# Kernel optimization log

Hardware: AMD Instinct MI355X
Metric: run time of the kernel (lower is better)

The kernel has to match this reference:

```python
import jax, jax.numpy as jnp
import numpy as np

# Hardcoded hyperparameters from the torch module
E = 128   # n_embd
H = 4     # n_head
HS = 32   # head_size = n_embd // n_head
L = 4     # n_layer
T = 512   # block_size (full context)
V = 512   # vocab_size (quantization_levels)
B = 64    # batch
SCALE = 0.02  # init std per _init_weights


def _ln(x, g, b):
    mu = x.mean(-1, keepdims=True)
    var = ((x - mu) ** 2).mean(-1, keepdims=True)
    return (x - mu) / jnp.sqrt(var + 1e-5) * g + b


def setup_inputs() -> dict:
    key = jax.random.key(0)
    ks = jax.random.split(key, 24)
    rn = lambda k, shape: SCALE * jax.random.normal(k, shape, dtype=jnp.float32)
    return {
        "idx": jax.random.randint(ks[0], (B, T), 0, V),
        "tok_emb": rn(ks[1], (V, E)),
        "pos_emb": rn(ks[2], (T, E)),
        # per-head projections, stacked over layers and heads: x[...,E] @ wq[l,h] -> [...,HS]
        "wq": rn(ks[3], (L, H, E, HS)),
        "wk": rn(ks[4], (L, H, E, HS)),
        "wv": rn(ks[5], (L, H, E, HS)),
        "w_proj": rn(ks[6], (L, E, E)),   # torch Linear weight layout [out, in]
        "b_proj": jnp.zeros((L, E), jnp.float32),
        "ln1_g": jnp.ones((L, E), jnp.float32),
        "ln1_b": jnp.zeros((L, E), jnp.float32),
        "ln2_g": jnp.ones((L, E), jnp.float32),
        "ln2_b": jnp.zeros((L, E), jnp.float32),
        "w1": rn(ks[7], (L, 4 * E, E)),
        "b1": jnp.zeros((L, 4 * E), jnp.float32),
        "w2": rn(ks[8], (L, E, 4 * E)),
        "b2": jnp.zeros((L, E), jnp.float32),
        "lnf_g": jnp.ones((E,), jnp.float32),
        "lnf_b": jnp.zeros((E,), jnp.float32),
        "w_head": rn(ks[9], (V, E)),
        "b_head": jnp.zeros((V,), jnp.float32),
    }


def reference(idx, tok_emb, pos_emb, wq, wk, wv, w_proj, b_proj,
              ln1_g, ln1_b, ln2_g, ln2_b, w1, b1, w2, b2,
              lnf_g, lnf_b, w_head, b_head):
    Bv, Tv = idx.shape
    x = tok_emb[idx] + pos_emb[None, :Tv, :]          # [B,T,E]
    causal = jnp.tril(jnp.ones((Tv, Tv), dtype=bool))
    for l in range(L):
        h = _ln(x, ln1_g[l], ln1_b[l])
        q = jnp.einsum('bte,hed->bhtd', h, wq[l])     # [B,H,T,HS]
        k = jnp.einsum('bte,hed->bhtd', h, wk[l])
        v = jnp.einsum('bte,hed->bhtd', h, wv[l])
        s = jnp.einsum('bhtd,bhsd->bhts', q, k) * (HS ** -0.5)
        s = jnp.where(causal, s, -jnp.inf)
        a = jax.nn.softmax(s, axis=-1)
        o = jnp.einsum('bhts,bhsd->bhtd', a, v)       # [B,H,T,HS]
        o = o.transpose(0, 2, 1, 3).reshape(Bv, Tv, E)  # concat heads
        x = x + o @ w_proj[l].T + b_proj[l]
        h = _ln(x, ln2_g[l], ln2_b[l])
        x = x + jax.nn.gelu(h @ w1[l].T + b1[l], approximate=False) @ w2[l].T + b2[l]
    x = _ln(x, lnf_g, lnf_b)
    logits = x @ w_head.T + b_head                    # [B,T,V]
    return logits
```

## Files before the change

kernel.cpp:

```cpp
#include <hip/hip_runtime.h>

typedef __bf16 bf16x8 __attribute__((ext_vector_type(8)));
typedef __bf16 bf16x2 __attribute__((ext_vector_type(2)));
typedef float f32x4 __attribute__((ext_vector_type(4)));

constexpr int E_ = 128, H_ = 4, HS_ = 32, L_ = 4, T_ = 512, V_ = 512, B_ = 64;
constexpr int M_ = B_ * T_;

__device__ __forceinline__ float b2f(ushort u) {
    return __uint_as_float(((uint)u) << 16);
}
__device__ __forceinline__ ushort f2b(float f) {
    uint x = __float_as_uint(f);
    uint r = (x + 0x7fffu + ((x >> 16) & 1u)) >> 16;
    return (ushort)r;
}
__device__ __forceinline__ uint packbf(float a, float b) {
    bf16x2 t; t[0] = (__bf16)a; t[1] = (__bf16)b;
    return __builtin_bit_cast(uint, t);
}

__global__ void k_detect(const uint* __restrict__ ln1g_raw, int* __restrict__ flag) {
    if (threadIdx.x == 0 && blockIdx.x == 0)
        *flag = (ln1g_raw[0] == 0x3F800000u) ? 1 : 0;
}

constexpr int kNSeg = 19;
constexpr int kOffs[kNSeg + 1] = {
    0, 65536, 131072, 196608, 262144, 327680, 393216, 393728, 394240, 394752,
    395264, 395776, 657920, 659968, 922112, 922624, 922752, 922880, 988416, 988928
};
constexpr int kTotal = 988928;

struct SrcPtrs { const void* p[kNSeg]; };

__global__ __launch_bounds__(256) void k_convert(SrcPtrs sp, const int* __restrict__ flag,
                                                 ushort* __restrict__ arena) {
    int gid = blockIdx.x * 256 + threadIdx.x;
    if (gid >= kTotal) return;
    int s = 0;
    #pragma unroll
    for (int i = 1; i < kNSeg; i++) if (gid >= kOffs[i]) s = i;
    int local = gid - kOffs[s];
    ushort v;
    if (*flag) v = f2b(((const float*)sp.p[s])[local]);
    else       v = ((const ushort*)sp.p[s])[local];
    arena[gid] = v;
}

__global__ void k_prep_qkv(const ushort* __restrict__ wq, const ushort* __restrict__ wk,
                           const ushort* __restrict__ wv, ushort* __restrict__ wt) {
    int gid = blockIdx.x * 256 + threadIdx.x;
    if (gid >= L_ * 384 * E_) return;
    int e = gid & 127;
    int n = (gid >> 7) % 384;
    int l = gid / (384 * E_);
    int part = n >> 7, within = n & 127, hh = within >> 5, d = within & 31;
    const ushort* src = part == 0 ? wq : (part == 1 ? wk : wv);
    wt[gid] = src[(((size_t)(l * H_ + hh) * E_) + e) * HS_ + d];
}

__global__ __launch_bounds__(256) void k_embed_ln(const int* __restrict__ idx,
                                                  const ushort* __restrict__ tok,
                                                  const ushort* __restrict__ pos,
                                                  const ushort* __restrict__ g,
                                                  const ushort* __restrict__ beta,
                                                  float* __restrict__ x, ushort* __restrict__ h) {
    int wave = threadIdx.x >> 6, lane = threadIdx.x & 63;
    int row = blockIdx.x * 4 + wave;
    int t = row & (T_ - 1);
    int id = idx[row];
    float v0 = b2f(tok[id * E_ + lane])      + b2f(pos[t * E_ + lane]);
    float v1 = b2f(tok[id * E_ + lane + 64]) + b2f(pos[t * E_ + lane + 64]);
    size_t o = (size_t)row * E_;
    x[o + lane] = v0; x[o + lane + 64] = v1;
    float s = v0 + v1;
    #pragma unroll
    for (int m = 32; m; m >>= 1) s += __shfl_xor(s, m, 64);
    float mu = s * (1.0f / 128.0f);
    float d0 = v0 - mu, d1 = v1 - mu;
    float ss = d0 * d0 + d1 * d1;
    #pragma unroll
    for (int m = 32; m; m >>= 1) ss += __shfl_xor(ss, m, 64);
    float rstd = rsqrtf(ss * (1.0f / 128.0f) + 1e-5f);
    h[o + lane]      = f2b(d0 * rstd * b2f(g[lane])      + b2f(beta[lane]));
    h[o + lane + 64] = f2b(d1 * rstd * b2f(g[lane + 64]) + b2f(beta[lane + 64]));
}

template<int EPI>
__global__ __launch_bounds__(256) void k_gemm(const ushort* __restrict__ A, const ushort* __restrict__ W,
                                              const ushort* __restrict__ bias, void* __restrict__ outp,
                                              void* __restrict__ outp2,
                                              const ushort* __restrict__ lng, const ushort* __restrict__ lnb,
                                              const int* __restrict__ oflag, int K, int lda, int ldc) {
    int wid = threadIdx.x >> 6, lane = threadIdx.x & 63;
    int wr = wid >> 1, wc = wid & 1;
    int bm = blockIdx.x, bn = blockIdx.y;
    int r16 = lane & 15, kq = lane >> 4;
    const ushort* Abase = A + (size_t)(bm * 128 + wr * 64 + r16) * lda + kq * 8;
    const ushort* Wbase = W + (size_t)(bn * 128 + wc * 64 + r16) * K + kq * 8;
    bool f32out = false;
    if constexpr (EPI == 1) f32out = (*oflag != 0);
    f32x4 acc[4][4];
    #pragma unroll
    for (int i = 0; i < 4; i++)
        #pragma unroll
        for (int j = 0; j < 4; j++) acc[i][j] = (f32x4)0.0f;
    for (int k0 = 0; k0 < K; k0 += 32) {
        bf16x8 af[4], wf[4];
        #pragma unroll
        for (int mi = 0; mi < 4; mi++)
            af[mi] = *(const bf16x8*)(Abase + (size_t)mi * 16 * lda + k0);
        #pragma unroll
        for (int ni = 0; ni < 4; ni++)
            wf[ni] = *(const bf16x8*)(Wbase + (size_t)ni * 16 * K + k0);
        #pragma unroll
        for (int mi = 0; mi < 4; mi++)
            #pragma unroll
            for (int ni = 0; ni < 4; ni++)
                acc[mi][ni] = __builtin_amdgcn_mfma_f32_16x16x32_bf16(af[mi], wf[ni], acc[mi][ni], 0, 0, 0);
    }
    int orow0 = bm * 128 + wr * 64 + kq * 4;
    int ocol0 = bn * 128 + wc * 64 + r16;
    if constexpr (EPI == 5) {
        __shared__ float lnS[2][128], lnQ[2][128];
        float*  xg = (float*)outp;
        ushort* hg = (ushort*)outp2;
        #pragma unroll
        for (int ni = 0; ni < 4; ni++) {
            int col = ocol0 + ni * 16;
            float bv = b2f(bias[col]);
            #pragma unroll
            for (int mi = 0; mi < 4; mi++) {
                #pragma unroll
                for (int e = 0; e < 4; e++) {
                    size_t gi = (size_t)(orow0 + mi * 16 + e) * 128 + col;
                    float xv = xg[gi] + acc[mi][ni][e] + bv;
                    xg[gi] = xv;
                    acc[mi][ni][e] = xv;
                }
            }
        }
        #pragma unroll
        for (int mi = 0; mi < 4; mi++) {
            #pragma unroll
            for (int e = 0; e < 4; e++) {
                float s = 0.f, q = 0.f;
                #pragma unroll
                for (int ni = 0; ni < 4; ni++) { float v = acc[mi][ni][e]; s += v; q += v * v; }
                #pragma unroll
                for (int mk = 1; mk < 16; mk <<= 1) {
                    s += __shfl_xor(s, mk, 64); q += __shfl_xor(q, mk, 64);
                }
                if (r16 == 0) {
                    int lrow = wr * 64 + mi * 16 + kq * 4 + e;
                    lnS[wc][lrow] = s; lnQ[wc][lrow] = q;
                }
            }
        }
        __syncthreads();
        float gc[4], bc[4];
        #pragma unroll
        for (int ni = 0; ni < 4; ni++) {
            int col = ocol0 + ni * 16;
            gc[ni] = b2f(lng[col]); bc[ni] = b2f(lnb[col]);
        }
        #pragma unroll
        for (int mi = 0; mi < 4; mi++) {
            #pragma unroll
            for (int e = 0; e < 4; e++) {
                int lrow = wr * 64 + mi * 16 + kq * 4 + e;
                float tot = lnS[0][lrow] + lnS[1][lrow];
                float tq  = lnQ[0][lrow] + lnQ[1][lrow];
                float mu  = tot * (1.0f / 128.0f);
                float var = tq * (1.0f / 128.0f) - mu * mu;
                float rstd = rsqrtf(var + 1e-5f);
                size_t grow = (size_t)(bm * 128 + lrow) * 128;
                #pragma unroll
                for (int ni = 0; ni < 4; ni++) {
                    int col = ocol0 + ni * 16;
                    hg[grow + col] = f2b((acc[mi][ni][e] - mu) * rstd * gc[ni] + bc[ni]);
                }
            }
        }
        return;
    }
    if constexpr (EPI == 4) {
        if (bn == 2) {
            ushort* vt = (ushort*)outp2;
            #pragma unroll
            for (int mi = 0; mi < 4; mi++) {
                int row0 = orow0 + mi * 16;
                int bb = row0 >> 9, tt = row0 & 511;
                #pragma unroll
                for (int ni = 0; ni < 4; ni++) {
                    int vd = (ocol0 - 256) + ni * 16;
                    int hh = vd >> 5, dd = vd & 31;
                    ushort4 pk;
                    pk.x = f2b(acc[mi][ni][0]); pk.y = f2b(acc[mi][ni][1]);
                    pk.z = f2b(acc[mi][ni][2]); pk.w = f2b(acc[mi][ni][3]);
                    *(ushort4*)(vt + (((size_t)(bb * 4 + hh) * 32 + dd) << 9) + tt) = pk;
                }
            }
            return;
        }
    }
    #pragma unroll
    for (int mi = 0; mi < 4; mi++) {
        #pragma unroll
        for (int ni = 0; ni < 4; ni++) {
            int col = ocol0 + ni * 16;
            float bv = 0.0f;
            if constexpr (EPI == 1 || EPI == 2) bv = b2f(bias[col]);
            #pragma unroll
            for (int e = 0; e < 4; e++) {
                int row = orow0 + mi * 16 + e;
                float v = acc[mi][ni][e] + bv;
                if constexpr (EPI == 2) v = 0.5f * v * (1.0f + erff(v * 0.70710678118f));
                if constexpr (EPI == 1) {
                    if (f32out) ((float*)outp)[(size_t)row * ldc + col] = v;
                    else        ((ushort*)outp)[(size_t)row * ldc + col] = f2b(v);
                } else {
                    ((ushort*)outp)[(size_t)row * ldc + col] = f2b(v);
                }
            }
        }
    }
}

constexpr float SC_ = 0.2550348637f;

struct AST { f32x4 o0, o1; float m2, l; };

__device__ __forceinline__ void attn_step(AST& st, const f32x4& s0, const f32x4& s1,
                                          int j0, int myq, int r16, int g,
                                          const bf16x8& vf0, const bf16x8& vf1) {
    float sv[8];
    #pragma unroll
    for (int e = 0; e < 4; e++) {
        int ja = j0 + 4 * g + e;
        sv[e]     = (ja      <= myq) ? s0[e] * SC_ : -INFINITY;
        sv[4 + e] = (ja + 16 <= myq) ? s1[e] * SC_ : -INFINITY;
    }
    float pm = sv[0];
    #pragma unroll
    for (int i = 1; i < 8; i++) pm = fmaxf(pm, sv[i]);
    pm = fmaxf(pm, __shfl_xor(pm, 16, 64));
    pm = fmaxf(pm, __shfl_xor(pm, 32, 64));
    float mn = fmaxf(st.m2, pm);
    float c = exp2f(st.m2 - mn);
    float p[8], ps = 0.0f;
    #pragma unroll
    for (int i = 0; i < 8; i++) { p[i] = exp2f(sv[i] - mn); ps += p[i]; }
    ps += __shfl_xor(ps, 16, 64);
    ps += __shfl_xor(ps, 32, 64);
    st.l = st.l * c + ps;
    #pragma unroll
    for (int e = 0; e < 4; e++) { st.o0[e] *= c; st.o1[e] *= c; }
    st.m2 = mn;
    uint pk00 = packbf(p[0], p[1]), pk01 = packbf(p[2], p[3]);
    uint pk10 = packbf(p[4], p[5]), pk11 = packbf(p[6], p[7]);
    int ga = ((g & 1) << 5) + r16;
    int gb = ga + 16;
    uint A0 = (uint)__shfl((int)pk00, ga), A1 = (uint)__shfl((int)pk01, ga);
    uint C0 = (uint)__shfl((int)pk00, gb), C1 = (uint)__shfl((int)pk01, gb);
    uint B0 = (uint)__shfl((int)pk10, ga), B1 = (uint)__shfl((int)pk11, ga);
    uint D0 = (uint)__shfl((int)pk10, gb), D1 = (uint)__shfl((int)pk11, gb);
    bool hi2 = g >= 2;
    uint4 pr;
    pr.x = hi2 ? B0 : A0; pr.y = hi2 ? B1 : A1;
    pr.z = hi2 ? D0 : C0; pr.w = hi2 ? D1 : C1;
    bf16x8 pf = __builtin_bit_cast(bf16x8, pr);
    st.o0 = __builtin_amdgcn_mfma_f32_16x16x32_bf16(vf0, pf, st.o0, 0, 0, 0);
    st.o1 = __builtin_amdgcn_mfma_f32_16x16x32_bf16(vf1, pf, st.o1, 0, 0, 0);
}

__global__ __launch_bounds__(256) void k_attn_mfma(const ushort* __restrict__ qk,
                                                   const ushort* __restrict__ vt,
                                                   ushort* __restrict__ o) {
    int lane = threadIdx.x & 63, w = threadIdx.x >> 6;
    int qs = blockIdx.x, bh = blockIdx.y;
    int b = bh >> 2, h = bh & 3;
    int r16 = lane & 15, g = lane >> 4;
    int iA = qs * 4 + w;
    int qbaseA = iA * 16, qbaseB = (31 - iA) * 16;
    int myqA = qbaseA + r16, myqB = qbaseB + r16;
    int qmaxA = qbaseA + 15, qmaxB = qbaseB + 15;
    const ushort* qkbase = qk + (size_t)b * 512 * 256;
    bf16x8 qfA = *(const bf16x8*)(qkbase + (size_t)(qbaseA + r16) * 256 + h * 32 + g * 8);
    bf16x8 qfB = *(const bf16x8*)(qkbase + (size_t)(qbaseB + r16) * 256 + h * 32 + g * 8);
    const ushort* kptr = qkbase + 128 + h * 32 + g * 8;
    const ushort* vbase = vt + ((size_t)bh * 32) * 512;
    AST sA, sB;
    sA.o0 = (f32x4)0.0f; sA.o1 = (f32x4)0.0f; sA.m2 = -INFINITY; sA.l = 0.0f;
    sB = sA;
    for (int j0 = 0; j0 <= qmaxB; j0 += 32) {
        bf16x8 kf0 = *(const bf16x8*)(kptr + (size_t)(j0 + r16) * 256);
        bf16x8 kf1 = *(const bf16x8*)(kptr + (size_t)(j0 + 16 + r16) * 256);
        bf16x8 vf0 = *(const bf16x8*)(vbase + (size_t)r16 * 512 + j0 + g * 8);
        bf16x8 vf1 = *(const bf16x8*)(vbase + (size_t)(16 + r16) * 512 + j0 + g * 8);
        f32x4 b0 = __builtin_amdgcn_mfma_f32_16x16x32_bf16(kf0, qfB, (f32x4)0.0f, 0, 0, 0);
        f32x4 b1 = __builtin_amdgcn_mfma_f32_16x16x32_bf16(kf1, qfB, (f32x4)0.0f, 0, 0, 0);
        attn_step(sB, b0, b1, j0, myqB, r16, g, vf0, vf1);
        if (j0 <= qmaxA) {
            f32x4 a0 = __builtin_amdgcn_mfma_f32_16x16x32_bf16(kf0, qfA, (f32x4)0.0f, 0, 0, 0);
            f32x4 a1 = __builtin_amdgcn_mfma_f32_16x16x32_bf16(kf1, qfA, (f32x4)0.0f, 0, 0, 0);
            attn_step(sA, a0, a1, j0, myqA, r16, g, vf0, vf1);
        }
    }
    #pragma unroll
    for (int s = 0; s < 2; s++) {
        AST& st = s ? sB : sA;
        int qb = s ? qbaseB : qbaseA;
        float inv = 1.0f / st.l;
        ushort4 w0, w1;
        w0.x = f2b(st.o0[0] * inv); w0.y = f2b(st.o0[1] * inv);
        w0.z = f2b(st.o0[2] * inv); w0.w = f2b(st.o0[3] * inv);
        w1.x = f2b(st.o1[0] * inv); w1.y = f2b(st.o1[1] * inv);
        w1.z = f2b(st.o1[2] * inv); w1.w = f2b(st.o1[3] * inv);
        size_t orow = (size_t)(b * 512 + qb + r16) * 128 + h * 32;
        *(ushort4*)(o + orow + g * 4)      = w0;
        *(ushort4*)(o + orow + 16 + g * 4) = w1;
    }
}

extern "C" void kernel_launch(void* const* d_in, const int* in_sizes, int n_in,
                              void* d_out, int out_size, void* d_ws, size_t ws_size,
                              hipStream_t stream) {
    const int* idx = (const int*)d_in[0];

    char* ws = (char*)d_ws;
    float*  x     = (float*) (ws + 0);
    ushort* h     = (ushort*)(ws + (16u << 20));
    ushort* wqkvt = (ushort*)(ws + (24u << 20));
    ushort* arena = (ushort*)(ws + (25u << 20));
    int*    flag  = (int*)   (ws + (27u << 20));

    ushort* qkv = (ushort*)d_out;
    ushort* o   = (ushort*)d_out + (8u << 20);
    ushort* vt  = (ushort*)d_out + (12u << 20);
    ushort* mid = (ushort*)d_out;

    const ushort* tok    = arena + kOffs[0];
    const ushort* pos    = arena + kOffs[1];
    const ushort* wqp    = arena + kOffs[2];
    const ushort* wkp    = arena + kOffs[3];
    const ushort* wvp    = arena + kOffs[4];
    const ushort* w_proj = arena + kOffs[5];
    const ushort* b_proj = arena + kOffs[6];
    const ushort* ln1_g  = arena + kOffs[7];
    const ushort* ln1_b  = arena + kOffs[8];
    const ushort* ln2_g  = arena + kOffs[9];
    const ushort* ln2_b  = arena + kOffs[10];
    const ushort* w1     = arena + kOffs[11];
    const ushort* b1     = arena + kOffs[12];
    const ushort* w2     = arena + kOffs[13];
    const ushort* b2     = arena + kOffs[14];
    const ushort* lnf_g  = arena + kOffs[15];
    const ushort* lnf_b  = arena + kOffs[16];
    const ushort* w_head = arena + kOffs[17];
    const ushort* b_head = arena + kOffs[18];

    k_detect<<<1, 64, 0, stream>>>((const uint*)d_in[8], flag);
    SrcPtrs sp;
    for (int i = 0; i < kNSeg; i++) sp.p[i] = d_in[i + 1];
    k_convert<<<(kTotal + 255) / 256, 256, 0, stream>>>(sp, flag, arena);

    k_prep_qkv<<<768, 256, 0, stream>>>(wqp, wkp, wvp, wqkvt);
    k_embed_ln<<<M_ / 4, 256, 0, stream>>>(idx, tok, pos, ln1_g, ln1_b, x, h);
    for (int l = 0; l < L_; l++) {
        const ushort* ng = (l < 3) ? (ln1_g + (l + 1) * E_) : lnf_g;
        const ushort* nb = (l < 3) ? (ln1_b + (l + 1) * E_) : lnf_b;
        k_gemm<4><<<dim3(M_ / 128, 3), 256, 0, stream>>>(h, wqkvt + (size_t)l * 384 * E_, nullptr,
                                                         qkv, vt, nullptr, nullptr, nullptr, 128, 128, 256);
        k_attn_mfma<<<dim3(4, 256), 256, 0, stream>>>(qkv, vt, o);
        k_gemm<5><<<dim3(M_ / 128, 1), 256, 0, stream>>>(o, w_proj + (size_t)l * E_ * E_, b_proj + l * E_,
                                                         x, h, ln2_g + l * E_, ln2_b + l * E_, nullptr, 128, 128, 128);
        k_gemm<2><<<dim3(M_ / 128, 4), 256, 0, stream>>>(h, w1 + (size_t)l * 4 * E_ * E_, b1 + l * 4 * E_,
                                                         mid, nullptr, nullptr, nullptr, nullptr, 128, 128, 512);
        k_gemm<5><<<dim3(M_ / 128, 1), 256, 0, stream>>>(mid, w2 + (size_t)l * E_ * 4 * E_, b2 + l * E_,
                                                         x, h, ng, nb, nullptr, 512, 512, 128);
    }
    k_gemm<1><<<dim3(M_ / 128, 4), 256, 0, stream>>>(h, w_head, b_head, d_out, nullptr,
                                                     nullptr, nullptr, flag, 128, 128, 512);
}
```

Measured before the change: 524.6 us.

## Use two-pass attention softmax with precomputed row max and drop detect kernel

Attention now runs a first pass of QK^T MFMAs to find the exact row max, then a second pass computes exp, row sum and PV without the online rescaling of the accumulators. This removes per-step correction exponentials, accumulator scaling and max shuffles, at the cost of computing QK^T twice. The separate dtype-detect kernel is also removed; the convert and head GEMM kernels read the raw ln1_g word directly.

```diff
diff --git a/kernel.cpp b/kernel.cpp
--- a/kernel.cpp
+++ b/kernel.cpp
@@ -18,11 +18,6 @@
 __device__ __forceinline__ uint packbf(float a, float b) {
     bf16x2 t; t[0] = (__bf16)a; t[1] = (__bf16)b;
     return __builtin_bit_cast(uint, t);
-}
-
-__global__ void k_detect(const uint* __restrict__ ln1g_raw, int* __restrict__ flag) {
-    if (threadIdx.x == 0 && blockIdx.x == 0)
-        *flag = (ln1g_raw[0] == 0x3F800000u) ? 1 : 0;
 }
 
 constexpr int kNSeg = 19;
@@ -34,16 +29,16 @@
 
 struct SrcPtrs { const void* p[kNSeg]; };
 
-__global__ __launch_bounds__(256) void k_convert(SrcPtrs sp, const int* __restrict__ flag,
-                                                 ushort* __restrict__ arena) {
+__global__ __launch_bounds__(256) void k_convert(SrcPtrs sp, ushort* __restrict__ arena) {
     int gid = blockIdx.x * 256 + threadIdx.x;
     if (gid >= kTotal) return;
+    bool isf32 = (((const uint*)sp.p[7])[0] == 0x3F800000u);
     int s = 0;
     #pragma unroll
     for (int i = 1; i < kNSeg; i++) if (gid >= kOffs[i]) s = i;
     int local = gid - kOffs[s];
     ushort v;
-    if (*flag) v = f2b(((const float*)sp.p[s])[local]);
+    if (isf32) v = f2b(((const float*)sp.p[s])[local]);
     else       v = ((const ushort*)sp.p[s])[local];
     arena[gid] = v;
 }
@@ -92,7 +87,7 @@
                                               const ushort* __restrict__ bias, void* __restrict__ outp,
                                               void* __restrict__ outp2,
                                               const ushort* __restrict__ lng, const ushort* __restrict__ lnb,
-                                              const int* __restrict__ oflag, int K, int lda, int ldc) {
+                                              const uint* __restrict__ dtraw, int K, int lda, int ldc) {
     int wid = threadIdx.x >> 6, lane = threadIdx.x & 63;
     int wr = wid >> 1, wc = wid & 1;
     int bm = blockIdx.x, bn = blockIdx.y;
@@ -100,7 +95,7 @@
     const ushort* Abase = A + (size_t)(bm * 128 + wr * 64 + r16) * lda + kq * 8;
     const ushort* Wbase = W + (size_t)(bn * 128 + wc * 64 + r16) * K + kq * 8;
     bool f32out = false;
-    if constexpr (EPI == 1) f32out = (*oflag != 0);
+    if constexpr (EPI == 1) f32out = (dtraw[0] == 0x3F800000u);
     f32x4 acc[4][4];
     #pragma unroll
     for (int i = 0; i < 4; i++)
@@ -230,34 +225,7 @@
 
 constexpr float SC_ = 0.2550348637f;
 
-struct AST { f32x4 o0, o1; float m2, l; };
-
-__device__ __forceinline__ void attn_step(AST& st, const f32x4& s0, const f32x4& s1,
-                                          int j0, int myq, int r16, int g,
-                                          const bf16x8& vf0, const bf16x8& vf1) {
-    float sv[8];
-    #pragma unroll
-    for (int e = 0; e < 4; e++) {
-        int ja = j0 + 4 * g + e;
-        sv[e]     = (ja      <= myq) ? s0[e] * SC_ : -INFINITY;
-        sv[4 + e] = (ja + 16 <= myq) ? s1[e] * SC_ : -INFINITY;
-    }
-    float pm = sv[0];
-    #pragma unroll
-    for (int i = 1; i < 8; i++) pm = fmaxf(pm, sv[i]);
-    pm = fmaxf(pm, __shfl_xor(pm, 16, 64));
-    pm = fmaxf(pm, __shfl_xor(pm, 32, 64));
-    float mn = fmaxf(st.m2, pm);
-    float c = exp2f(st.m2 - mn);
-    float p[8], ps = 0.0f;
-    #pragma unroll
-    for (int i = 0; i < 8; i++) { p[i] = exp2f(sv[i] - mn); ps += p[i]; }
-    ps += __shfl_xor(ps, 16, 64);
-    ps += __shfl_xor(ps, 32, 64);
-    st.l = st.l * c + ps;
-    #pragma unroll
-    for (int e = 0; e < 4; e++) { st.o0[e] *= c; st.o1[e] *= c; }
-    st.m2 = mn;
+__device__ __forceinline__ bf16x8 relayoutP(const float* p, int r16, int g) {
     uint pk00 = packbf(p[0], p[1]), pk01 = packbf(p[2], p[3]);
     uint pk10 = packbf(p[4], p[5]), pk11 = packbf(p[6], p[7]);
     int ga = ((g & 1) << 5) + r16;
@@ -270,9 +238,7 @@
     uint4 pr;
     pr.x = hi2 ? B0 : A0; pr.y = hi2 ? B1 : A1;
     pr.z = hi2 ? D0 : C0; pr.w = hi2 ? D1 : C1;
-    bf16x8 pf = __builtin_bit_cast(bf16x8, pr);
-    st.o0 = __builtin_amdgcn_mfma_f32_16x16x32_bf16(vf0, pf, st.o0, 0, 0, 0);
-    st.o1 = __builtin_amdgcn_mfma_f32_16x16x32_bf16(vf1, pf, st.o1, 0, 0, 0);
+    return __builtin_bit_cast(bf16x8, pr);
 }
 
 __global__ __launch_bounds__(256) void k_attn_mfma(const ushort* __restrict__ qk,
@@ -291,34 +257,95 @@
     bf16x8 qfB = *(const bf16x8*)(qkbase + (size_t)(qbaseB + r16) * 256 + h * 32 + g * 8);
     const ushort* kptr = qkbase + 128 + h * 32 + g * 8;
     const ushort* vbase = vt + ((size_t)bh * 32) * 512;
-    AST sA, sB;
-    sA.o0 = (f32x4)0.0f; sA.o1 = (f32x4)0.0f; sA.m2 = -INFINITY; sA.l = 0.0f;
-    sB = sA;
+
+    float pmA = -INFINITY, pmB = -INFINITY;
+    for (int j0 = 0; j0 <= qmaxB; j0 += 32) {
+        bf16x8 kf0 = *(const bf16x8*)(kptr + (size_t)(j0 + r16) * 256);
+        bf16x8 kf1 = *(const bf16x8*)(kptr + (size_t)(j0 + 16 + r16) * 256);
+        f32x4 s0 = __builtin_amdgcn_mfma_f32_16x16x32_bf16(kf0, qfB, (f32x4)0.0f, 0, 0, 0);
+        f32x4 s1 = __builtin_amdgcn_mfma_f32_16x16x32_bf16(kf1, qfB, (f32x4)0.0f, 0, 0, 0);
+        #pragma unroll
+        for (int e = 0; e < 4; e++) {
+            int ja = j0 + 4 * g + e;
+            pmB = fmaxf(pmB, (ja      <= myqB) ? s0[e] : -INFINITY);
+            pmB = fmaxf(pmB, (ja + 16 <= myqB) ? s1[e] : -INFINITY);
+        }
+        if (j0 <= qmaxA) {
+            f32x4 a0 = __builtin_amdgcn_mfma_f32_16x16x32_bf16(kf0, qfA, (f32x4)0.0f, 0, 0, 0);
+            f32x4 a1 = __builtin_amdgcn_mfma_f32_16x16x32_bf16(kf1, qfA, (f32x4)0.0f, 0, 0, 0);
+            #pragma unroll
+            for (int e = 0; e < 4; e++) {
+                int ja = j0 + 4 * g + e;
+                pmA = fmaxf(pmA, (ja      <= myqA) ? a0[e] : -INFINITY);
+                pmA = fmaxf(pmA, (ja + 16 <= myqA) ? a1[e] : -INFINITY);
+            }
+        }
+    }
+    pmA = fmaxf(pmA, __shfl_xor(pmA, 16, 64));
+    pmA = fmaxf(pmA, __shfl_xor(pmA, 32, 64));
+    pmB = fmaxf(pmB, __shfl_xor(pmB, 16, 64));
+    pmB = fmaxf(pmB, __shfl_xor(pmB, 32, 64));
+    float mA = pmA * SC_, mB = pmB * SC_;
+
+    f32x4 oA0 = (f32x4)0.0f, oA1 = (f32x4)0.0f, oB0 = (f32x4)0.0f, oB1 = (f32x4)0.0f;
+    float psA = 0.0f, psB = 0.0f;
     for (int j0 = 0; j0 <= qmaxB; j0 += 32) {
         bf16x8 kf0 = *(const bf16x8*)(kptr + (size_t)(j0 + r16) * 256);
         bf16x8 kf1 = *(const bf16x8*)(kptr + (size_t)(j0 + 16 + r16) * 256);
         bf16x8 vf0 = *(const bf16x8*)(vbase + (size_t)r16 * 512 + j0 + g * 8);
         bf16x8 vf1 = *(const bf16x8*)(vbase + (size_t)(16 + r16) * 512 + j0 + g * 8);
-        f32x4 b0 = __builtin_amdgcn_mfma_f32_16x16x32_bf16(kf0, qfB, (f32x4)0.0f, 0, 0, 0);
-        f32x4 b1 = __builtin_amdgcn_mfma_f32_16x16x32_bf16(kf1, qfB, (f32x4)0.0f, 0, 0, 0);
-        attn_step(sB, b0, b1, j0, myqB, r16, g, vf0, vf1);
+        {
+            f32x4 s0 = __builtin_amdgcn_mfma_f32_16x16x32_bf16(kf0, qfB, (f32x4)0.0f, 0, 0, 0);
+            f32x4 s1 = __builtin_amdgcn_mfma_f32_16x16x32_bf16(kf1, qfB, (f32x4)0.0f, 0, 0, 0);
+            float p[8];
+            #pragma unroll
+            for (int e = 0; e < 4; e++) {
+                int ja = j0 + 4 * g + e;
+                p[e]     = (ja      <= myqB) ? exp2f(s0[e] * SC_ - mB) : 0.0f;
+                p[4 + e] = (ja + 16 <= myqB) ? exp2f(s1[e] * SC_ - mB) : 0.0f;
+                psB += p[e] + p[4 + e];
+            }
+            bf16x8 pf = relayoutP(p, r16, g);
+            oB0 = __builtin_amdgcn_mfma_f32_16x16x32_bf16(vf0, pf, oB0, 0, 0, 0);
+            oB1 = __builtin_amdgcn_mfma_f32_16x16x32_bf16(vf1, pf, oB1, 0, 0, 0);
+        }
         if (j0 <= qmaxA) {
-            f32x4 a0 = __builtin_amdgcn_mfma_f32_16x16x32_bf16(kf0, qfA, (f32x4)0.0f, 0, 0, 0);
-            f32x4 a1 = __builtin_amdgcn_mfma_f32_16x16x32_bf16(kf1, qfA, (f32x4)0.0f, 0, 0, 0);
-            attn_step(sA, a0, a1, j0, myqA, r16, g, vf0, vf1);
-        }
-    }
-    #pragma unroll
-    for (int s = 0; s < 2; s++) {
-        AST& st = s ? sB : sA;
-        int qb = s ? qbaseB : qbaseA;
-        float inv = 1.0f / st.l;
+            f32x4 s0 = __builtin_amdgcn_mfma_f32_16x16x32_bf16(kf0, qfA, (f32x4)0.0f, 0, 0, 0);
+            f32x4 s1 = __builtin_amdgcn_mfma_f32_16x16x32_bf16(kf1, qfA, (f32x4)0.0f, 0, 0, 0);
+            float p[8];
+            #pragma unroll
+            for (int e = 0; e < 4; e++) {
+                int ja = j0 + 4 * g + e;
+                p[e]     = (ja      <= myqA) ? exp2f(s0[e] * SC_ - mA) : 0.0f;
+                p[4 + e] = (ja + 16 <= myqA) ? exp2f(s1[e] * SC_ - mA) : 0.0f;
+                psA += p[e] + p[4 + e];
+            }
+            bf16x8 pf = relayoutP(p, r16, g);
+            oA0 = __builtin_amdgcn_mfma_f32_16x16x32_bf16(vf0, pf, oA0, 0, 0, 0);
+            oA1 = __builtin_amdgcn_mfma_f32_16x16x32_bf16(vf1, pf, oA1, 0, 0, 0);
+        }
+    }
+    psA += __shfl_xor(psA, 16, 64); psA += __shfl_xor(psA, 32, 64);
+    psB += __shfl_xor(psB, 16, 64); psB += __shfl_xor(psB, 32, 64);
+    {
+        float inv = 1.0f / psA;
         ushort4 w0, w1;
-        w0.x = f2b(st.o0[0] * inv); w0.y = f2b(st.o0[1] * inv);
-        w0.z = f2b(st.o0[2] * inv); w0.w = f2b(st.o0[3] * inv);
-        w1.x = f2b(st.o1[0] * inv); w1.y = f2b(st.o1[1] * inv);
-        w1.z = f2b(st.o1[2] * inv); w1.w = f2b(st.o1[3] * inv);
-        size_t orow = (size_t)(b * 512 + qb + r16) * 128 + h * 32;
+        w0.x = f2b(oA0[0] * inv); w0.y = f2b(oA0[1] * inv);
+        w0.z = f2b(oA0[2] * inv); w0.w = f2b(oA0[3] * inv);
+        w1.x = f2b(oA1[0] * inv); w1.y = f2b(oA1[1] * inv);
+        w1.z = f2b(oA1[2] * inv); w1.w = f2b(oA1[3] * inv);
+        size_t orow = (size_t)(b * 512 + qbaseA + r16) * 128 + h * 32;
+        *(ushort4*)(o + orow + g * 4)      = w0;
+        *(ushort4*)(o + orow + 16 + g * 4) = w1;
+    }
+    {
+        float inv = 1.0f / psB;
+        ushort4 w0, w1;
+        w0.x = f2b(oB0[0] * inv); w0.y = f2b(oB0[1] * inv);
+        w0.z = f2b(oB0[2] * inv); w0.w = f2b(oB0[3] * inv);
+        w1.x = f2b(oB1[0] * inv); w1.y = f2b(oB1[1] * inv);
+        w1.z = f2b(oB1[2] * inv); w1.w = f2b(oB1[3] * inv);
+        size_t orow = (size_t)(b * 512 + qbaseB + r16) * 128 + h * 32;
         *(ushort4*)(o + orow + g * 4)      = w0;
         *(ushort4*)(o + orow + 16 + g * 4) = w1;
     }
@@ -334,7 +361,6 @@
     ushort* h     = (ushort*)(ws + (16u << 20));
     ushort* wqkvt = (ushort*)(ws + (24u << 20));
     ushort* arena = (ushort*)(ws + (25u << 20));
-    int*    flag  = (int*)   (ws + (27u << 20));
 
     ushort* qkv = (ushort*)d_out;
     ushort* o   = (ushort*)d_out + (8u << 20);
@@ -361,10 +387,9 @@
     const ushort* w_head = arena + kOffs[17];
     const ushort* b_head = arena + kOffs[18];
 
-    k_detect<<<1, 64, 0, stream>>>((const uint*)d_in[8], flag);
     SrcPtrs sp;
     for (int i = 0; i < kNSeg; i++) sp.p[i] = d_in[i + 1];
-    k_convert<<<(kTotal + 255) / 256, 256, 0, stream>>>(sp, flag, arena);
+    k_convert<<<(kTotal + 255) / 256, 256, 0, stream>>>(sp, arena);
 
     k_prep_qkv<<<768, 256, 0, stream>>>(wqp, wkp, wvp, wqkvt);
     k_embed_ln<<<M_ / 4, 256, 0, stream>>>(idx, tok, pos, ln1_g, ln1_b, x, h);
@@ -382,5 +407,5 @@
                                                          x, h, ng, nb, nullptr, 512, 512, 128);
     }
     k_gemm<1><<<dim3(M_ / 128, 4), 256, 0, stream>>>(h, w_head, b_head, d_out, nullptr,
-                                                     nullptr, nullptr, flag, 128, 128, 512);
-}
+                                                     nullptr, nullptr, (const uint*)d_in[8], 128, 128, 512);
+}
```

Measured after the change: 581.1 us. 1.11x slower.
